# Performance work log

Hardware: AMD Instinct MI355X
Metric: run time of the kernel (lower is better)

Reference implementation:

```python
import jax, jax.numpy as jnp
import numpy as np

IN_FEATURES = 100000
OUT_FEATURES = 100000
NNZ = 1600000
BATCH = 64


def setup_inputs() -> dict:
    key = jax.random.key(0)
    k1, k2, k3, k4, k5 = jax.random.split(key, 5)
    x = jax.random.normal(k1, (BATCH, IN_FEATURES), dtype=jnp.float32)
    values = jax.random.normal(k2, (NNZ,), dtype=jnp.float32)
    bias = jax.random.normal(k3, (OUT_FEATURES,), dtype=jnp.float32)
    # torch COO is coalesced -> row indices sorted (rows = dst of transposed matrix)
    rows = jnp.sort(jax.random.randint(k4, (NNZ,), 0, OUT_FEATURES, dtype=jnp.int64))
    cols = jax.random.randint(k5, (NNZ,), 0, IN_FEATURES, dtype=jnp.int64)
    return {"x": x, "values": values, "bias": bias, "rows": rows, "cols": cols}


def reference(x, values, bias, rows, cols):
    # out = x @ conn  <=>  out.T = conn_T @ x.T, conn_T given in COO (rows=dst, cols=src)
    # gather source activations along edges: (nnz, B)
    contrib = x[:, cols].T * values[:, None]
    # scatter-add into destinations: (out_features, B)
    out_t = jax.ops.segment_sum(contrib, rows, num_segments=OUT_FEATURES,
                                indices_are_sorted=True)
    return out_t.T + bias  # (B, out_features)
```

## Files before the change

kernel.cpp:

```cpp
#include <hip/hip_runtime.h>
#include <hip/hip_fp16.h>

#define IN_F   100000
#define OUT_F  100000
#define NNZ_N  1600000
#define TC     256
#define TBLK   ((IN_F + TC - 1) / TC)
#define SBLK   ((NNZ_N + 255) / 256)

__device__ __forceinline__ float2 h2f(unsigned u) {
    const __half2 h = *reinterpret_cast<const __half2*>(&u);
    return __half22float2(h);
}

__global__ __launch_bounds__(256) void k_prep(
    const float* __restrict__ x,
    const int*   __restrict__ rows,
    const int*   __restrict__ cols,
    const float* __restrict__ vals,
    unsigned* __restrict__ xh,
    int*      __restrict__ rstart,
    uint2*    __restrict__ pairs) {
    __shared__ unsigned tile[TC][33];
    const int bid = blockIdx.x;
    const int t   = threadIdx.x;

    if (bid < TBLK) {
        const int i0   = bid * TC;
        const int colr = i0 + t;
        if (colr < IN_F) {
            #pragma unroll 8
            for (int p = 0; p < 32; ++p) {
                const float a = x[(size_t)(2 * p)     * IN_F + colr];
                const float b = x[(size_t)(2 * p + 1) * IN_F + colr];
                const __half2 h = __floats2half2_rn(a, b);
                tile[t][p] = *reinterpret_cast<const unsigned*>(&h);
            }
        }
        __syncthreads();
        const int u  = t & 31;
        const int c8 = t >> 5;
        for (int cc = c8; cc < TC; cc += 8) {
            const int col = i0 + cc;
            if (col < IN_F)
                xh[(size_t)col * 32 + u] = tile[cc][u];
        }
    } else {
        const int e = (bid - TBLK) * 256 + t;
        if (e >= NNZ_N) return;
        const int cur  = rows[e];
        const int prev = (e == 0) ? -1 : rows[e - 1];
        for (int r = prev + 1; r <= cur; ++r) rstart[r] = e;
        if (e == NNZ_N - 1)
            for (int r = cur + 1; r <= OUT_F; ++r) rstart[r] = NNZ_N;
        pairs[e] = make_uint2((unsigned)cols[e], __float_as_uint(vals[e]));
    }
}

__global__ __launch_bounds__(512, 4) void k_spmm(
    const uint4* __restrict__ xh4,
    const uint2* __restrict__ pairs,
    const int*   __restrict__ rstart_g,
    const float* __restrict__ bias,
    float* __restrict__ out) {
    __shared__ int   rs[65];
    __shared__ float tile[64][65];
    const int r0   = blockIdx.x * 64;
    const int t    = threadIdx.x;
    const int lane = t & 63;
    const int w    = t >> 6;

    if (t < 65) {
        int idx = r0 + t; if (idx > OUT_F) idx = OUT_F;
        rs[t] = rstart_g[idx];
    }
    __syncthreads();

    const int g   = lane >> 3;
    const int sub = lane & 7;
    const int lj  = (w << 3) + g;
    const int s   = rs[lj];
    const int e   = rs[lj + 1];

    float acc[8];
    #pragma unroll
    for (int i = 0; i < 8; ++i) acc[i] = 0.f;

    for (int base = s; base < e; base += 4) {
        const int e1 = e - 1;
        const int i1 = (base + 1 < e) ? base + 1 : e1;
        const int i2 = (base + 2 < e) ? base + 2 : e1;
        const int i3 = (base + 3 < e) ? base + 3 : e1;
        const uint2 p0 = pairs[base];
        const uint2 p1 = pairs[i1];
        const uint2 p2 = pairs[i2];
        const uint2 p3 = pairs[i3];
        const float v0 = __uint_as_float(p0.y);
        const float v1 = (base + 1 < e) ? __uint_as_float(p1.y) : 0.f;
        const float v2 = (base + 2 < e) ? __uint_as_float(p2.y) : 0.f;
        const float v3 = (base + 3 < e) ? __uint_as_float(p3.y) : 0.f;
        const uint4 u0 = xh4[(size_t)p0.x * 8 + sub];
        const uint4 u1 = xh4[(size_t)p1.x * 8 + sub];
        const uint4 u2 = xh4[(size_t)p2.x * 8 + sub];
        const uint4 u3 = xh4[(size_t)p3.x * 8 + sub];
        float2 f;
        f = h2f(u0.x); acc[0] = fmaf(v0, f.x, acc[0]); acc[1] = fmaf(v0, f.y, acc[1]);
        f = h2f(u0.y); acc[2] = fmaf(v0, f.x, acc[2]); acc[3] = fmaf(v0, f.y, acc[3]);
        f = h2f(u0.z); acc[4] = fmaf(v0, f.x, acc[4]); acc[5] = fmaf(v0, f.y, acc[5]);
        f = h2f(u0.w); acc[6] = fmaf(v0, f.x, acc[6]); acc[7] = fmaf(v0, f.y, acc[7]);
        f = h2f(u1.x); acc[0] = fmaf(v1, f.x, acc[0]); acc[1] = fmaf(v1, f.y, acc[1]);
        f = h2f(u1.y); acc[2] = fmaf(v1, f.x, acc[2]); acc[3] = fmaf(v1, f.y, acc[3]);
        f = h2f(u1.z); acc[4] = fmaf(v1, f.x, acc[4]); acc[5] = fmaf(v1, f.y, acc[5]);
        f = h2f(u1.w); acc[6] = fmaf(v1, f.x, acc[6]); acc[7] = fmaf(v1, f.y, acc[7]);
        f = h2f(u2.x); acc[0] = fmaf(v2, f.x, acc[0]); acc[1] = fmaf(v2, f.y, acc[1]);
        f = h2f(u2.y); acc[2] = fmaf(v2, f.x, acc[2]); acc[3] = fmaf(v2, f.y, acc[3]);
        f = h2f(u2.z); acc[4] = fmaf(v2, f.x, acc[4]); acc[5] = fmaf(v2, f.y, acc[5]);
        f = h2f(u2.w); acc[6] = fmaf(v2, f.x, acc[6]); acc[7] = fmaf(v2, f.y, acc[7]);
        f = h2f(u3.x); acc[0] = fmaf(v3, f.x, acc[0]); acc[1] = fmaf(v3, f.y, acc[1]);
        f = h2f(u3.y); acc[2] = fmaf(v3, f.x, acc[2]); acc[3] = fmaf(v3, f.y, acc[3]);
        f = h2f(u3.z); acc[4] = fmaf(v3, f.x, acc[4]); acc[5] = fmaf(v3, f.y, acc[5]);
        f = h2f(u3.w); acc[6] = fmaf(v3, f.x, acc[6]); acc[7] = fmaf(v3, f.y, acc[7]);
    }

    #pragma unroll
    for (int i = 0; i < 8; ++i) tile[lj][(sub << 3) + i] = acc[i];
    __syncthreads();

    const int rc = r0 + lane;
    if (rc < OUT_F) {
        const float bv = bias[rc];
        for (int bb = w; bb < 64; bb += 8)
            out[(size_t)bb * OUT_F + rc] = tile[lane][bb] + bv;
    }
}

__global__ __launch_bounds__(256) void k_spmm_fallback(
    const float* __restrict__ x,
    const float* __restrict__ vals,
    const int*   __restrict__ rows,
    const int*   __restrict__ cols,
    const float* __restrict__ bias,
    float* __restrict__ out) {
    __shared__ int   rstart[65];
    __shared__ float tile[64][65];
    const int r0   = blockIdx.x * 64;
    const int t    = threadIdx.x;
    const int lane = t & 63;
    const int w    = t >> 6;
    if (t < 65) {
        const int target = r0 + t;
        int lo = 0, hi = NNZ_N;
        while (lo < hi) {
            const int mid = (lo + hi) >> 1;
            if (rows[mid] < target) lo = mid + 1; else hi = mid;
        }
        rstart[t] = lo;
    }
    __syncthreads();
    for (int j = w; j < 64; j += 4) {
        const int s = rstart[j], e = rstart[j + 1];
        float acc = 0.f;
        const size_t base = (size_t)lane * IN_F;
        for (int idx = s; idx < e; ++idx)
            acc = fmaf(vals[idx], x[base + cols[idx]], acc);
        tile[j][lane] = acc;
    }
    __syncthreads();
    const int c = lane;
    if (r0 + c < OUT_F) {
        const float bv = bias[r0 + c];
        for (int bb = w; bb < 64; bb += 4)
            out[(size_t)bb * OUT_F + (r0 + c)] = tile[c][bb] + bv;
    }
}

extern "C" void kernel_launch(void* const* d_in, const int* in_sizes, int n_in,
                              void* d_out, int out_size, void* d_ws, size_t ws_size,
                              hipStream_t stream) {
    const float* x      = (const float*)d_in[0];
    const float* values = (const float*)d_in[1];
    const float* bias   = (const float*)d_in[2];
    const int*   rows   = (const int*)d_in[3];
    const int*   cols   = (const int*)d_in[4];
    float*       out    = (float*)d_out;

    const size_t xh_bytes = (size_t)IN_F * 32 * sizeof(unsigned);
    const size_t rs_off   = (xh_bytes + 255) & ~(size_t)255;
    const size_t rs_bytes = (size_t)(OUT_F + 1) * sizeof(int);
    const size_t pr_off   = (rs_off + rs_bytes + 255) & ~(size_t)255;
    const size_t need     = pr_off + (size_t)NNZ_N * sizeof(uint2);

    const int row_blocks = (OUT_F + 63) / 64;

    if (ws_size >= need) {
        unsigned* xh     = (unsigned*)d_ws;
        int*      rstart = (int*)((char*)d_ws + rs_off);
        uint2*    pairs  = (uint2*)((char*)d_ws + pr_off);
        k_prep<<<TBLK + SBLK, 256, 0, stream>>>(x, rows, cols, values, xh, rstart, pairs);
        k_spmm<<<row_blocks, 512, 0, stream>>>(
            (const uint4*)xh, pairs, rstart, bias, out);
    } else {
        k_spmm_fallback<<<row_blocks, 256, 0, stream>>>(x, values, rows, cols, bias, out);
    }
}
```

Measured before the change: 131.5 us.

## Assign two adjacent output rows per 8-lane group to balance nnz work

Each 8-lane group now walks the combined edge range of two consecutive output rows and routes each edge's value into one of two accumulator sets, selected by comparing against the row boundary. Blocks now cover 128 rows, so the grid has half as many blocks. The aim is to lengthen each group's loop and smooth out uneven row lengths, cutting tail-iteration waste and divergence between groups. In exchange every edge does twice the FMAs, since the unused set gets a zero weight, register use goes up, and there are fewer blocks to fill the GPU.

```diff
diff --git a/kernel.cpp b/kernel.cpp
--- a/kernel.cpp
+++ b/kernel.cpp
@@ -63,14 +63,14 @@
     const int*   __restrict__ rstart_g,
     const float* __restrict__ bias,
     float* __restrict__ out) {
-    __shared__ int   rs[65];
-    __shared__ float tile[64][65];
-    const int r0   = blockIdx.x * 64;
+    __shared__ int   rs[129];
+    __shared__ float tile[128][65];
+    const int r0   = blockIdx.x * 128;
     const int t    = threadIdx.x;
     const int lane = t & 63;
     const int w    = t >> 6;
 
-    if (t < 65) {
+    if (t < 129) {
         int idx = r0 + t; if (idx > OUT_F) idx = OUT_F;
         rs[t] = rstart_g[idx];
     }
@@ -78,19 +78,22 @@
 
     const int g   = lane >> 3;
     const int sub = lane & 7;
-    const int lj  = (w << 3) + g;
-    const int s   = rs[lj];
-    const int e   = rs[lj + 1];
-
-    float acc[8];
+    const int gid = (w << 3) + g;
+    const int lj0 = gid << 1;
+
+    const int s = rs[lj0];
+    const int m = rs[lj0 + 1];
+    const int e = rs[lj0 + 2];
+
+    float acc0[8], acc1[8];
     #pragma unroll
-    for (int i = 0; i < 8; ++i) acc[i] = 0.f;
+    for (int i = 0; i < 8; ++i) { acc0[i] = 0.f; acc1[i] = 0.f; }
 
     for (int base = s; base < e; base += 4) {
-        const int e1 = e - 1;
-        const int i1 = (base + 1 < e) ? base + 1 : e1;
-        const int i2 = (base + 2 < e) ? base + 2 : e1;
-        const int i3 = (base + 3 < e) ? base + 3 : e1;
+        const int eL = e - 1;
+        const int i1 = (base + 1 < e) ? base + 1 : eL;
+        const int i2 = (base + 2 < e) ? base + 2 : eL;
+        const int i3 = (base + 3 < e) ? base + 3 : eL;
         const uint2 p0 = pairs[base];
         const uint2 p1 = pairs[i1];
         const uint2 p2 = pairs[i2];
@@ -99,38 +102,65 @@
         const float v1 = (base + 1 < e) ? __uint_as_float(p1.y) : 0.f;
         const float v2 = (base + 2 < e) ? __uint_as_float(p2.y) : 0.f;
         const float v3 = (base + 3 < e) ? __uint_as_float(p3.y) : 0.f;
+        const float a0 = (base     < m) ? v0 : 0.f, b0 = (base     < m) ? 0.f : v0;
+        const float a1 = (base + 1 < m) ? v1 : 0.f, b1 = (base + 1 < m) ? 0.f : v1;
+        const float a2 = (base + 2 < m) ? v2 : 0.f, b2 = (base + 2 < m) ? 0.f : v2;
+        const float a3 = (base + 3 < m) ? v3 : 0.f, b3 = (base + 3 < m) ? 0.f : v3;
         const uint4 u0 = xh4[(size_t)p0.x * 8 + sub];
         const uint4 u1 = xh4[(size_t)p1.x * 8 + sub];
         const uint4 u2 = xh4[(size_t)p2.x * 8 + sub];
         const uint4 u3 = xh4[(size_t)p3.x * 8 + sub];
         float2 f;
-        f = h2f(u0.x); acc[0] = fmaf(v0, f.x, acc[0]); acc[1] = fmaf(v0, f.y, acc[1]);
-        f = h2f(u0.y); acc[2] = fmaf(v0, f.x, acc[2]); acc[3] = fmaf(v0, f.y, acc[3]);
-        f = h2f(u0.z); acc[4] = fmaf(v0, f.x, acc[4]); acc[5] = fmaf(v0, f.y, acc[5]);
-        f = h2f(u0.w); acc[6] = fmaf(v0, f.x, acc[6]); acc[7] = fmaf(v0, f.y, acc[7]);
-        f = h2f(u1.x); acc[0] = fmaf(v1, f.x, acc[0]); acc[1] = fmaf(v1, f.y, acc[1]);
-        f = h2f(u1.y); acc[2] = fmaf(v1, f.x, acc[2]); acc[3] = fmaf(v1, f.y, acc[3]);
-        f = h2f(u1.z); acc[4] = fmaf(v1, f.x, acc[4]); acc[5] = fmaf(v1, f.y, acc[5]);
-        f = h2f(u1.w); acc[6] = fmaf(v1, f.x, acc[6]); acc[7] = fmaf(v1, f.y, acc[7]);
-        f = h2f(u2.x); acc[0] = fmaf(v2, f.x, acc[0]); acc[1] = fmaf(v2, f.y, acc[1]);
-        f = h2f(u2.y); acc[2] = fmaf(v2, f.x, acc[2]); acc[3] = fmaf(v2, f.y, acc[3]);
-        f = h2f(u2.z); acc[4] = fmaf(v2, f.x, acc[4]); acc[5] = fmaf(v2, f.y, acc[5]);
-        f = h2f(u2.w); acc[6] = fmaf(v2, f.x, acc[6]); acc[7] = fmaf(v2, f.y, acc[7]);
-        f = h2f(u3.x); acc[0] = fmaf(v3, f.x, acc[0]); acc[1] = fmaf(v3, f.y, acc[1]);
-        f = h2f(u3.y); acc[2] = fmaf(v3, f.x, acc[2]); acc[3] = fmaf(v3, f.y, acc[3]);
-        f = h2f(u3.z); acc[4] = fmaf(v3, f.x, acc[4]); acc[5] = fmaf(v3, f.y, acc[5]);
-        f = h2f(u3.w); acc[6] = fmaf(v3, f.x, acc[6]); acc[7] = fmaf(v3, f.y, acc[7]);
+        f = h2f(u0.x); acc0[0] = fmaf(a0, f.x, acc0[0]); acc1[0] = fmaf(b0, f.x, acc1[0]);
+                       acc0[1] = fmaf(a0, f.y, acc0[1]); acc1[1] = fmaf(b0, f.y, acc1[1]);
+        f = h2f(u0.y); acc0[2] = fmaf(a0, f.x, acc0[2]); acc1[2] = fmaf(b0, f.x, acc1[2]);
+                       acc0[3] = fmaf(a0, f.y, acc0[3]); acc1[3] = fmaf(b0, f.y, acc1[3]);
+        f = h2f(u0.z); acc0[4] = fmaf(a0, f.x, acc0[4]); acc1[4] = fmaf(b0, f.x, acc1[4]);
+                       acc0[5] = fmaf(a0, f.y, acc0[5]); acc1[5] = fmaf(b0, f.y, acc1[5]);
+        f = h2f(u0.w); acc0[6] = fmaf(a0, f.x, acc0[6]); acc1[6] = fmaf(b0, f.x, acc1[6]);
+                       acc0[7] = fmaf(a0, f.y, acc0[7]); acc1[7] = fmaf(b0, f.y, acc1[7]);
+        f = h2f(u1.x); acc0[0] = fmaf(a1, f.x, acc0[0]); acc1[0] = fmaf(b1, f.x, acc1[0]);
+                       acc0[1] = fmaf(a1, f.y, acc0[1]); acc1[1] = fmaf(b1, f.y, acc1[1]);
+        f = h2f(u1.y); acc0[2] = fmaf(a1, f.x, acc0[2]); acc1[2] = fmaf(b1, f.x, acc1[2]);
+                       acc0[3] = fmaf(a1, f.y, acc0[3]); acc1[3] = fmaf(b1, f.y, acc1[3]);
+        f = h2f(u1.z); acc0[4] = fmaf(a1, f.x, acc0[4]); acc1[4] = fmaf(b1, f.x, acc1[4]);
+                       acc0[5] = fmaf(a1, f.y, acc0[5]); acc1[5] = fmaf(b1, f.y, acc1[5]);
+        f = h2f(u1.w); acc0[6] = fmaf(a1, f.x, acc0[6]); acc1[6] = fmaf(b1, f.x, acc1[6]);
+                       acc0[7] = fmaf(a1, f.y, acc0[7]); acc1[7] = fmaf(b1, f.y, acc1[7]);
+        f = h2f(u2.x); acc0[0] = fmaf(a2, f.x, acc0[0]); acc1[0] = fmaf(b2, f.x, acc1[0]);
+                       acc0[1] = fmaf(a2, f.y, acc0[1]); acc1[1] = fmaf(b2, f.y, acc1[1]);
+        f = h2f(u2.y); acc0[2] = fmaf(a2, f.x, acc0[2]); acc1[2] = fmaf(b2, f.x, acc1[2]);
+                       acc0[3] = fmaf(a2, f.y, acc0[3]); acc1[3] = fmaf(b2, f.y, acc1[3]);
+        f = h2f(u2.z); acc0[4] = fmaf(a2, f.x, acc0[4]); acc1[4] = fmaf(b2, f.x, acc1[4]);
+                       acc0[5] = fmaf(a2, f.y, acc0[5]); acc1[5] = fmaf(b2, f.y, acc1[5]);
+        f = h2f(u2.w); acc0[6] = fmaf(a2, f.x, acc0[6]); acc1[6] = fmaf(b2, f.x, acc1[6]);
+                       acc0[7] = fmaf(a2, f.y, acc0[7]); acc1[7] = fmaf(b2, f.y, acc1[7]);
+        f = h2f(u3.x); acc0[0] = fmaf(a3, f.x, acc0[0]); acc1[0] = fmaf(b3, f.x, acc1[0]);
+                       acc0[1] = fmaf(a3, f.y, acc0[1]); acc1[1] = fmaf(b3, f.y, acc1[1]);
+        f = h2f(u3.y); acc0[2] = fmaf(a3, f.x, acc0[2]); acc1[2] = fmaf(b3, f.x, acc1[2]);
+                       acc0[3] = fmaf(a3, f.y, acc0[3]); acc1[3] = fmaf(b3, f.y, acc1[3]);
+        f = h2f(u3.z); acc0[4] = fmaf(a3, f.x, acc0[4]); acc1[4] = fmaf(b3, f.x, acc1[4]);
+                       acc0[5] = fmaf(a3, f.y, acc0[5]); acc1[5] = fmaf(b3, f.y, acc1[5]);
+        f = h2f(u3.w); acc0[6] = fmaf(a3, f.x, acc0[6]); acc1[6] = fmaf(b3, f.x, acc1[6]);
+                       acc0[7] = fmaf(a3, f.y, acc0[7]); acc1[7] = fmaf(b3, f.y, acc1[7]);
     }
 
     #pragma unroll
-    for (int i = 0; i < 8; ++i) tile[lj][(sub << 3) + i] = acc[i];
-    __syncthreads();
-
-    const int rc = r0 + lane;
-    if (rc < OUT_F) {
-        const float bv = bias[rc];
-        for (int bb = w; bb < 64; bb += 8)
-            out[(size_t)bb * OUT_F + rc] = tile[lane][bb] + bv;
+    for (int i = 0; i < 8; ++i) {
+        tile[lj0    ][(sub << 3) + i] = acc0[i];
+        tile[lj0 + 1][(sub << 3) + i] = acc1[i];
+    }
+    __syncthreads();
+
+    #pragma unroll
+    for (int half = 0; half < 2; ++half) {
+        const int lr = (half << 6) + lane;
+        const int rc = r0 + lr;
+        if (rc < OUT_F) {
+            const float bv = bias[rc];
+            for (int bb = w; bb < 64; bb += 8)
+                out[(size_t)bb * OUT_F + rc] = tile[lr][bb] + bv;
+        }
     }
 }
 
@@ -190,7 +220,7 @@
     const size_t pr_off   = (rs_off + rs_bytes + 255) & ~(size_t)255;
     const size_t need     = pr_off + (size_t)NNZ_N * sizeof(uint2);
 
-    const int row_blocks = (OUT_F + 63) / 64;
+    const int row_blocks = (OUT_F + 127) / 128;
 
     if (ws_size >= need) {
         unsigned* xh     = (unsigned*)d_ws;
@@ -200,6 +230,7 @@
         k_spmm<<<row_blocks, 512, 0, stream>>>(
             (const uint4*)xh, pairs, rstart, bias, out);
     } else {
-        k_spmm_fallback<<<row_blocks, 256, 0, stream>>>(x, values, rows, cols, bias, out);
-    }
-}
+        k_spmm_fallback<<<(OUT_F + 63) / 64, 256, 0, stream>>>(
+            x, values, rows, cols, bias, out);
+    }
+}
```

New measurement: 135.0 us. 2.7% more time.
